# Kernel tuning notes

Hardware: AMD Instinct MI355X
Metric: run time of the kernel (lower is better)

## Reference

```python
import jax, jax.numpy as jnp
import numpy as np

B = 16384          # number of graphs
NPG = 9            # nodes per graph (op_idx reshaped to B*9)
D = 128            # d_model
L = 4              # num_layers (GCN order)
EPG = 16           # random intra-graph edges per graph
LN_EPS = 1e-5


def setup_inputs() -> dict:
    key = jax.random.key(0)
    ks = jax.random.split(key, 12)
    op_idx = jax.random.randint(ks[0], (B, NPG), 0, 7)
    # edges strictly within each 9-node graph, offset per graph
    s = jax.random.randint(ks[1], (B, EPG), 0, NPG)
    t = jax.random.randint(ks[2], (B, EPG), 0, NPG)
    off = (jnp.arange(B) * NPG)[:, None]
    src = (s + off).reshape(-1)
    dst = (t + off).reshape(-1)
    f32 = jnp.float32
    op_table = jax.random.normal(ks[3], (7, D), f32)
    device_emb = jax.random.normal(ks[4], (1, D), f32)
    Wg = jax.random.normal(ks[5], (L, D, D), f32) / np.sqrt(D)
    bg = jnp.zeros((L, D), f32)
    ln_g = jnp.ones((L, D), f32)
    ln_b = jnp.zeros((L, D), f32)
    W1 = jax.random.normal(ks[6], (L, D, 4 * D), f32) / np.sqrt(D)
    b1 = jnp.zeros((L, 4 * D), f32)
    W2 = jax.random.normal(ks[7], (L, 4 * D, D), f32) / np.sqrt(4 * D)
    b2 = jnp.zeros((L, D), f32)
    fc_w = jax.random.normal(ks[8], (D, 1), f32) / np.sqrt(D)
    fc_b = jnp.zeros((1,), f32)
    return dict(op_table=op_table, device_emb=device_emb, Wg=Wg, bg=bg,
                ln_g=ln_g, ln_b=ln_b, W1=W1, b1=b1, W2=W2, b2=b2,
                fc_w=fc_w, fc_b=fc_b, op_idx=op_idx, src=src, dst=dst)


def _layer_norm(x, g, b):
    mu = x.mean(-1, keepdims=True)
    var = jnp.mean(jnp.square(x - mu), -1, keepdims=True)
    return (x - mu) * jax.lax.rsqrt(var + LN_EPS) * g + b


def reference(op_table, device_emb, Wg, bg, ln_g, ln_b, W1, b1, W2, b2,
              fc_w, fc_b, op_idx, src, dst):
    n_graphs = op_idx.shape[0]
    N = n_graphs * NPG
    # embedding lookup + broadcast add of device embedding: [N, D]
    h = op_table[op_idx].reshape(N, -1) + device_emb
    # add self loops
    loop = jnp.arange(N)
    s_all = jnp.concatenate([src, loop])
    d_all = jnp.concatenate([dst, loop])
    deg = jax.ops.segment_sum(jnp.ones_like(s_all, dtype=h.dtype), d_all,
                              num_segments=N)
    inv_sqrt_deg = jax.lax.rsqrt(jnp.maximum(deg, 1.0))
    enorm = (inv_sqrt_deg[s_all] * inv_sqrt_deg[d_all])[:, None]  # [E,1]
    n_layers = Wg.shape[0]
    for l in range(n_layers):
        # symmetric-normalized message passing (gather -> scale -> scatter-add)
        agg = jax.ops.segment_sum(h[s_all] * enorm, d_all, num_segments=N)
        h = jax.nn.relu(agg @ Wg[l] + bg[l])
        h = _layer_norm(h, ln_g[l], ln_b[l])
        h = h + jax.nn.relu(h @ W1[l] + b1[l]) @ W2[l] + b2[l]  # residual FFN
    # mean readout over the 9 nodes of each graph -> [B, D]
    g = h.reshape(n_graphs, NPG, -1).mean(axis=1)
    return jax.nn.sigmoid(g @ fc_w + fc_b)  # [B, 1]
```

## Files before the change

### kernel.cpp

```cpp
#include <hip/hip_runtime.h>

#define NGRAPH 16384
#define NPG    9
#define DM     128
#define NLAY   4
#define EPG    16
#define GPB    14
#define RPB    128
#define NBLK   1171
#define CBS    40
#define WPL    147456

typedef __attribute__((ext_vector_type(8))) short bf16x8;
typedef __attribute__((ext_vector_type(4))) float f32x4;
typedef __attribute__((ext_vector_type(2))) float f32x2;
typedef __attribute__((ext_vector_type(4))) unsigned int u32x4;

__device__ __forceinline__ float b2f(unsigned short u){
  union { unsigned int i; float f; } v; v.i = ((unsigned int)u) << 16; return v.f;
}
__device__ __forceinline__ unsigned short f2b(float f){
  union { float fv; unsigned int i; } v; v.fv = f;
  unsigned int r = v.i + 0x7FFFu + ((v.i >> 16) & 1u);
  return (unsigned short)(r >> 16);
}
__device__ __forceinline__ unsigned int cvt2(float lo, float hi){
  unsigned int r;
  asm("v_cvt_pk_bf16_f32 %0, %1, %2" : "=v"(r) : "v"(lo), "v"(hi));
  return r;
}
__device__ __forceinline__ float uasf(unsigned int u){
  union { unsigned int i; float f; } v; v.i = u; return v.f;
}

__device__ __forceinline__ bf16x8 ldfrag128(const unsigned short* buf, int row, int kk, int g16){
  return *(const bf16x8*)&buf[row*DM + ((kk*32 + g16*8) ^ ((row & 7) << 3))];
}
__device__ __forceinline__ f32x4 mfma16(bf16x8 a, bf16x8 b, f32x4 c){
  return __builtin_amdgcn_mfma_f32_16x16x32_bf16(a, b, c, 0, 0, 0);
}

__global__ void wtr_kernel(const float* __restrict__ Wg,
                           const float* __restrict__ W1,
                           const float* __restrict__ W2,
                           unsigned short* __restrict__ wsT){
  int idx = blockIdx.x * 256 + threadIdx.x;
  int e    = idx & 7;
  int lane = (idx >> 3) & 63;
  int f    = idx >> 9;
  int l = f / 288, s = f - l*288;
  int l15 = lane & 15, g16 = lane >> 4;
  float v;
  if (s < 32){
    int kk = s >> 3, nt = s & 7;
    v = Wg[l*16384 + (kk*32 + g16*8 + e)*128 + nt*16 + l15];
  } else if (s < 160){
    int s2 = s - 32; int c = s2 >> 3, fi = s2 & 7;
    int kk = fi >> 1, nt = fi & 1;
    v = W1[l*65536 + (kk*32 + g16*8 + e)*512 + c*32 + nt*16 + l15];
  } else {
    int s3 = s - 160; int c = s3 >> 3, nt = s3 & 7;
    v = W2[l*65536 + (c*32 + g16*8 + e)*128 + nt*16 + l15];
  }
  wsT[f*512 + lane*8 + e] = f2b(v);
}

__global__ void __launch_bounds__(256, 2)
gcn_kernel(const float* __restrict__ op_table,
           const float* __restrict__ dev_emb,
           const float* __restrict__ bgp,
           const float* __restrict__ lngp,
           const float* __restrict__ lnbp,
           const float* __restrict__ b1p,
           const float* __restrict__ b2p,
           const float* __restrict__ fcw,
           const float* __restrict__ fcb,
           const int* __restrict__ op_idx,
           const int* __restrict__ srcA,
           const int* __restrict__ dstA,
           const unsigned short* __restrict__ wsT,
           float* __restrict__ out)
{
  __shared__ unsigned short H[RPB*DM];
  __shared__ unsigned short Cb[RPB*CBS];
  __shared__ float cntF[GPB][81];
  __shared__ float isd_s[RPB];
  __shared__ float bg_s[DM], lng_s[DM], lnb_s[DM], b2_s[DM];
  __shared__ float b1_s[4*DM];

  const int tid  = threadIdx.x;
  const int w    = tid >> 6;
  const int lane = tid & 63;
  const int g16  = lane >> 4;
  const int l15  = lane & 15;
  const int rbase = w * 32;
  const int g0 = blockIdx.x * GPB;
  const int nvalid = (NGRAPH - g0 < GPB) ? (NGRAPH - g0) : GPB;

  for (int i = tid; i < GPB*81; i += 256) (&cntF[0][0])[i] = 0.f;

  {
    int r  = tid >> 1;
    int gh = (tid & 1) * 8;
    int gi = r / NPG;
    int j  = r - gi*NPG;
    if (r < GPB*NPG && gi < nvalid) {
      int idx = op_idx[(g0 + gi)*NPG + j];
      const float4* ot = (const float4*)&op_table[idx*DM + gh*8];
      const float4* de = (const float4*)&dev_emb[gh*8];
      #pragma unroll
      for (int i = 0; i < 8; ++i){
        float4 a0 = ot[2*i], a1 = ot[2*i+1];
        float4 d0 = de[2*i], d1 = de[2*i+1];
        u32x4 o;
        o[0] = cvt2(a0.x + d0.x, a0.y + d0.y);
        o[1] = cvt2(a0.z + d0.z, a0.w + d0.w);
        o[2] = cvt2(a1.x + d1.x, a1.y + d1.y);
        o[3] = cvt2(a1.z + d1.z, a1.w + d1.w);
        int g = gh + i;
        *(u32x4*)&H[r*DM + ((g ^ (r & 7)) << 3)] = o;
      }
    } else {
      u32x4 z; z[0]=z[1]=z[2]=z[3]=0u;
      #pragma unroll
      for (int i = 0; i < 8; ++i){
        int g = gh + i;
        *(u32x4*)&H[r*DM + ((g ^ (r & 7)) << 3)] = z;
      }
    }
  }
  __syncthreads();

  if (tid < GPB && tid < nvalid) {
    float* c = cntF[tid];
    for (int e = 0; e < EPG; ++e){
      int s = srcA[(g0 + tid)*EPG + e];
      int d = dstA[(g0 + tid)*EPG + e];
      c[(s % NPG)*NPG + (d % NPG)] += 1.f;
    }
    #pragma unroll
    for (int j = 0; j < NPG; ++j) c[j*NPG + j] += 1.f;
  }
  __syncthreads();

  if (tid < RPB) {
    int gi = tid / NPG;
    if (tid < GPB*NPG && gi < nvalid) {
      int jd = tid - gi*NPG;
      float s = 0.f;
      #pragma unroll
      for (int js = 0; js < NPG; ++js) s += cntF[gi][js*NPG + jd];
      isd_s[tid] = rsqrtf(s);
    } else isd_s[tid] = 1.f;
  }
  __syncthreads();

  for (int idx = tid; idx < GPB*81; idx += 256){
    int gi = idx / 81;
    int e  = idx - gi*81;
    int js = e / 9, jd = e - js*9;
    (&cntF[0][0])[idx] *= isd_s[gi*NPG + js] * isd_s[gi*NPG + jd];
  }
  __syncthreads();

  #pragma unroll 1
  for (int l = 0; l < NLAY; ++l){
    const unsigned short* WL = wsT + l*WPL;

    if (tid < DM) {
      bg_s[tid]  = bgp [l*DM + tid];
      lng_s[tid] = lngp[l*DM + tid];
      lnb_s[tid] = lnbp[l*DM + tid];
      b2_s[tid]  = b2p [l*DM + tid];
    }
    b1_s[tid]       = b1p[l*4*DM + tid];
    b1_s[tid + 256] = b1p[l*4*DM + 256 + tid];
    {
      int gi = tid >> 4;
      int g  = tid & 15;
      if (gi < GPB) {
        f32x2 hs[NPG][4];
        #pragma unroll
        for (int j = 0; j < NPG; ++j){
          int row = gi*NPG + j;
          u32x4 hv = *(const u32x4*)&H[row*DM + ((g ^ (row & 7)) << 3)];
          #pragma unroll
          for (int i = 0; i < 4; ++i){
            f32x2 t;
            t[0] = uasf(hv[i] << 16);
            t[1] = uasf(hv[i] & 0xffff0000u);
            hs[j][i] = t;
          }
        }
        #pragma unroll
        for (int jd = 0; jd < NPG; ++jd){
          f32x2 av[4];
          #pragma unroll
          for (int i = 0; i < 4; ++i){ f32x2 z; z[0]=0.f; z[1]=0.f; av[i]=z; }
          #pragma unroll
          for (int js = 0; js < NPG; ++js){
            float c = cntF[gi][js*NPG + jd];
            f32x2 cc; cc[0]=c; cc[1]=c;
            #pragma unroll
            for (int i = 0; i < 4; ++i)
              av[i] = __builtin_elementwise_fma(cc, hs[js][i], av[i]);
          }
          int row = gi*NPG + jd;
          u32x4 o;
          #pragma unroll
          for (int i = 0; i < 4; ++i) o[i] = cvt2(av[i][0], av[i][1]);
          *(u32x4*)&H[row*DM + ((g ^ (row & 7)) << 3)] = o;
        }
      } else {
        int k2 = tid - GPB*16;
        int row = GPB*NPG + (k2 >> 4);
        int gg = k2 & 15;
        u32x4 z; z[0]=z[1]=z[2]=z[3]=0u;
        *(u32x4*)&H[row*DM + ((gg ^ (row & 7)) << 3)] = z;
      }
    }
    __syncthreads();

    {
      const bf16x8* Bf = (const bf16x8*)WL;
      f32x4 acc[2][8];
      #pragma unroll
      for (int mt = 0; mt < 2; ++mt)
        #pragma unroll
        for (int nt = 0; nt < 8; ++nt){ f32x4 z; z[0]=z[1]=z[2]=z[3]=0.f; acc[mt][nt]=z; }
      #pragma unroll 2
      for (int kk = 0; kk < 4; ++kk){
        bf16x8 a0 = ldfrag128(H, rbase + l15, kk, g16);
        bf16x8 a1 = ldfrag128(H, rbase + 16 + l15, kk, g16);
        __builtin_amdgcn_s_setprio(1);
        #pragma unroll
        for (int nt = 0; nt < 8; ++nt){
          bf16x8 bb = Bf[(kk*8 + nt)*64 + lane];
          acc[0][nt] = mfma16(a0, bb, acc[0][nt]);
          acc[1][nt] = mfma16(a1, bb, acc[1][nt]);
        }
        __builtin_amdgcn_s_setprio(0);
      }
      #pragma unroll
      for (int mt = 0; mt < 2; ++mt){
        float rs[4], rq[4];
        #pragma unroll
        for (int j = 0; j < 4; ++j){ rs[j] = 0.f; rq[j] = 0.f; }
        #pragma unroll
        for (int nt = 0; nt < 8; ++nt){
          #pragma unroll
          for (int j = 0; j < 4; ++j){
            float v = acc[mt][nt][j] + bg_s[nt*16 + l15];
            v = fmaxf(v, 0.f);
            acc[mt][nt][j] = v;
            rs[j] += v; rq[j] += v*v;
          }
        }
        #pragma unroll
        for (int j = 0; j < 4; ++j){
          #pragma unroll
          for (int mm = 1; mm < 16; mm <<= 1){
            rs[j] += __shfl_xor(rs[j], mm, 64);
            rq[j] += __shfl_xor(rq[j], mm, 64);
          }
          float mu  = rs[j] * (1.f/128.f);
          float var = rq[j] * (1.f/128.f) - mu*mu;
          rs[j] = mu;
          rq[j] = rsqrtf(var + 1e-5f);
        }
        int rowb = rbase + mt*16 + g16*4;
        #pragma unroll
        for (int nt = 0; nt < 8; ++nt){
          int col = nt*16 + l15;
          float lg = lng_s[col], lb = lnb_s[col];
          float x0 = (acc[mt][nt][0] - rs[0]) * rq[0] * lg + lb;
          float x1 = (acc[mt][nt][1] - rs[1]) * rq[1] * lg + lb;
          float x2 = (acc[mt][nt][2] - rs[2]) * rq[2] * lg + lb;
          float x3 = (acc[mt][nt][3] - rs[3]) * rq[3] * lg + lb;
          unsigned int p01 = cvt2(x0, x1);
          unsigned int p23 = cvt2(x2, x3);
          int r0 = rowb, r1 = rowb+1, r2 = rowb+2, r3 = rowb+3;
          H[r0*DM + (col ^ ((r0 & 7) << 3))] = (unsigned short)p01;
          H[r1*DM + (col ^ ((r1 & 7) << 3))] = (unsigned short)(p01 >> 16);
          H[r2*DM + (col ^ ((r2 & 7) << 3))] = (unsigned short)p23;
          H[r3*DM + (col ^ ((r3 & 7) << 3))] = (unsigned short)(p23 >> 16);
        }
      }
    }

    {
      const unsigned short* W1b = WL + 16384;
      const unsigned short* W2b = WL + 81920;

      bf16x8 xa[8];
      #pragma unroll
      for (int kk = 0; kk < 4; ++kk){
        xa[kk*2 + 0] = ldfrag128(H, rbase + l15, kk, g16);
        xa[kk*2 + 1] = ldfrag128(H, rbase + 16 + l15, kk, g16);
      }

      f32x4 c2[2][8];
      #pragma unroll
      for (int mt = 0; mt < 2; ++mt)
        #pragma unroll
        for (int nt = 0; nt < 8; ++nt){ f32x4 z; z[0]=z[1]=z[2]=z[3]=0.f; c2[mt][nt]=z; }
      #pragma unroll 1
      for (int c = 0; c < 16; ++c){
        const bf16x8* B1 = (const bf16x8*)(W1b + c*4096);
        const bf16x8* B2 = (const bf16x8*)(W2b + c*4096);
        bf16x8 b1r[8], b2r[8];
        #pragma unroll
        for (int f = 0; f < 8; ++f) b1r[f] = B1[f*64 + lane];
        #pragma unroll
        for (int f = 0; f < 8; ++f) b2r[f] = B2[f*64 + lane];

        f32x4 hc[2][2];
        #pragma unroll
        for (int mt = 0; mt < 2; ++mt)
          #pragma unroll
          for (int nt = 0; nt < 2; ++nt){ f32x4 z; z[0]=z[1]=z[2]=z[3]=0.f; hc[mt][nt]=z; }
        __builtin_amdgcn_s_setprio(1);
        #pragma unroll
        for (int kk = 0; kk < 4; ++kk){
          #pragma unroll
          for (int nt = 0; nt < 2; ++nt){
            bf16x8 bb = b1r[kk*2 + nt];
            hc[0][nt] = mfma16(xa[kk*2 + 0], bb, hc[0][nt]);
            hc[1][nt] = mfma16(xa[kk*2 + 1], bb, hc[1][nt]);
          }
        }
        __builtin_amdgcn_s_setprio(0);
        #pragma unroll
        for (int mt = 0; mt < 2; ++mt){
          int rowb = rbase + mt*16 + g16*4;
          #pragma unroll
          for (int nt = 0; nt < 2; ++nt){
            int col = nt*16 + l15;
            float bv = b1_s[c*32 + col];
            float v0 = fmaxf(hc[mt][nt][0] + bv, 0.f);
            float v1 = fmaxf(hc[mt][nt][1] + bv, 0.f);
            float v2 = fmaxf(hc[mt][nt][2] + bv, 0.f);
            float v3 = fmaxf(hc[mt][nt][3] + bv, 0.f);
            unsigned int p01 = cvt2(v0, v1);
            unsigned int p23 = cvt2(v2, v3);
            Cb[(rowb + 0)*CBS + col] = (unsigned short)p01;
            Cb[(rowb + 1)*CBS + col] = (unsigned short)(p01 >> 16);
            Cb[(rowb + 2)*CBS + col] = (unsigned short)p23;
            Cb[(rowb + 3)*CBS + col] = (unsigned short)(p23 >> 16);
          }
        }
        {
          bf16x8 a0 = *(const bf16x8*)&Cb[(rbase + l15)*CBS + g16*8];
          bf16x8 a1 = *(const bf16x8*)&Cb[(rbase + 16 + l15)*CBS + g16*8];
          __builtin_amdgcn_s_setprio(1);
          #pragma unroll
          for (int nt = 0; nt < 8; ++nt){
            c2[0][nt] = mfma16(a0, b2r[nt], c2[0][nt]);
            c2[1][nt] = mfma16(a1, b2r[nt], c2[1][nt]);
          }
          __builtin_amdgcn_s_setprio(0);
        }
      }

      #pragma unroll
      for (int mt = 0; mt < 2; ++mt){
        int rowb = rbase + mt*16 + g16*4;
        #pragma unroll
        for (int nt = 0; nt < 8; ++nt){
          int col = nt*16 + l15;
          float b2v = b2_s[col];
          int p0 = (rowb+0)*DM + (col ^ (((rowb+0) & 7) << 3));
          int p1 = (rowb+1)*DM + (col ^ (((rowb+1) & 7) << 3));
          int p2 = (rowb+2)*DM + (col ^ (((rowb+2) & 7) << 3));
          int p3 = (rowb+3)*DM + (col ^ (((rowb+3) & 7) << 3));
          float s0 = b2f(H[p0]) + c2[mt][nt][0] + b2v;
          float s1 = b2f(H[p1]) + c2[mt][nt][1] + b2v;
          float s2 = b2f(H[p2]) + c2[mt][nt][2] + b2v;
          float s3 = b2f(H[p3]) + c2[mt][nt][3] + b2v;
          unsigned int p01 = cvt2(s0, s1);
          unsigned int p23 = cvt2(s2, s3);
          H[p0] = (unsigned short)p01;
          H[p1] = (unsigned short)(p01 >> 16);
          H[p2] = (unsigned short)p23;
          H[p3] = (unsigned short)(p23 >> 16);
        }
      }
    }
    __syncthreads();
  }

  {
    int gi = tid >> 4;
    int g  = tid & 15;
    if (gi < nvalid) {
      float m[8];
      #pragma unroll
      for (int i = 0; i < 8; ++i) m[i] = 0.f;
      #pragma unroll
      for (int j = 0; j < NPG; ++j){
        int row = gi*NPG + j;
        bf16x8 hv = *(const bf16x8*)&H[row*DM + ((g ^ (row & 7)) << 3)];
        #pragma unroll
        for (int i = 0; i < 8; ++i) m[i] += b2f((unsigned short)hv[i]);
      }
      const float4* fw = (const float4*)&fcw[g*8];
      float4 w0 = fw[0], w1 = fw[1];
      float dot = m[0]*w0.x + m[1]*w0.y + m[2]*w0.z + m[3]*w0.w
                + m[4]*w1.x + m[5]*w1.y + m[6]*w1.z + m[7]*w1.w;
      dot *= (1.f/9.f);
      #pragma unroll
      for (int mm = 1; mm < 16; mm <<= 1) dot += __shfl_xor(dot, mm, 64);
      if ((tid & 15) == 0){
        float z = dot + fcb[0];
        out[g0 + gi] = 1.f / (1.f + __expf(-z));
      }
    }
  }
}

extern "C" void kernel_launch(void* const* d_in, const int* in_sizes, int n_in,
                              void* d_out, int out_size, void* d_ws, size_t ws_size,
                              hipStream_t stream)
{
  const float* op_table = (const float*)d_in[0];
  const float* dev_emb  = (const float*)d_in[1];
  const float* Wg  = (const float*)d_in[2];
  const float* bg  = (const float*)d_in[3];
  const float* lng = (const float*)d_in[4];
  const float* lnb = (const float*)d_in[5];
  const float* W1  = (const float*)d_in[6];
  const float* b1  = (const float*)d_in[7];
  const float* W2  = (const float*)d_in[8];
  const float* b2  = (const float*)d_in[9];
  const float* fcw = (const float*)d_in[10];
  const float* fcb = (const float*)d_in[11];
  const int* op_idx = (const int*)d_in[12];
  const int* srcA   = (const int*)d_in[13];
  const int* dstA   = (const int*)d_in[14];
  unsigned short* wsT = (unsigned short*)d_ws;

  wtr_kernel<<<2304, 256, 0, stream>>>(Wg, W1, W2, wsT);
  gcn_kernel<<<NBLK, 256, 0, stream>>>(op_table, dev_emb, bg, lng, lnb, b1, b2,
                                       fcw, fcb, op_idx, srcA, dstA, wsT,
                                       (float*)d_out);
}
```

Baseline: 275.6 us.

## Prefetch layer weights into registers and double-buffer W1 chunks across FFN loop

Global loads of the GCN weight fragments are hoisted to the top of each layer, before the aggregation phase and barrier, so their latency overlaps the message-passing work. The FFN loop is unrolled by two, with W1 fragments double-buffered in registers (the even and odd chunks). The next chunk's W1 is loaded while the current chunk computes, and the first W1 chunk is prefetched during the LayerNorm epilogue. This raises register pressure considerably (32 extra bf16x8 for Wg plus 16 for W1), which could reduce occupancy or cause spills.

```diff
diff --git a/kernel.cpp b/kernel.cpp
--- a/kernel.cpp
+++ b/kernel.cpp
@@ -166,6 +166,11 @@
   #pragma unroll 1
   for (int l = 0; l < NLAY; ++l){
     const unsigned short* WL = wsT + l*WPL;
+    const bf16x8* Bg = (const bf16x8*)WL;
+
+    bf16x8 wg01[16];
+    #pragma unroll
+    for (int f = 0; f < 16; ++f) wg01[f] = Bg[f*64 + lane];
 
     if (tid < DM) {
       bg_s[tid]  = bgp [l*DM + tid];
@@ -221,26 +226,48 @@
     }
     __syncthreads();
 
+    bf16x8 b1E[8], b1O[8];
     {
-      const bf16x8* Bf = (const bf16x8*)WL;
+      bf16x8 wg23[16];
+      #pragma unroll
+      for (int f = 0; f < 16; ++f) wg23[f] = Bg[(16 + f)*64 + lane];
+
       f32x4 acc[2][8];
       #pragma unroll
       for (int mt = 0; mt < 2; ++mt)
         #pragma unroll
         for (int nt = 0; nt < 8; ++nt){ f32x4 z; z[0]=z[1]=z[2]=z[3]=0.f; acc[mt][nt]=z; }
-      #pragma unroll 2
-      for (int kk = 0; kk < 4; ++kk){
+      #pragma unroll
+      for (int kk = 0; kk < 2; ++kk){
         bf16x8 a0 = ldfrag128(H, rbase + l15, kk, g16);
         bf16x8 a1 = ldfrag128(H, rbase + 16 + l15, kk, g16);
         __builtin_amdgcn_s_setprio(1);
         #pragma unroll
         for (int nt = 0; nt < 8; ++nt){
-          bf16x8 bb = Bf[(kk*8 + nt)*64 + lane];
-          acc[0][nt] = mfma16(a0, bb, acc[0][nt]);
-          acc[1][nt] = mfma16(a1, bb, acc[1][nt]);
+          acc[0][nt] = mfma16(a0, wg01[kk*8 + nt], acc[0][nt]);
+          acc[1][nt] = mfma16(a1, wg01[kk*8 + nt], acc[1][nt]);
         }
         __builtin_amdgcn_s_setprio(0);
       }
+      #pragma unroll
+      for (int kk = 0; kk < 2; ++kk){
+        bf16x8 a0 = ldfrag128(H, rbase + l15, 2 + kk, g16);
+        bf16x8 a1 = ldfrag128(H, rbase + 16 + l15, 2 + kk, g16);
+        __builtin_amdgcn_s_setprio(1);
+        #pragma unroll
+        for (int nt = 0; nt < 8; ++nt){
+          acc[0][nt] = mfma16(a0, wg23[kk*8 + nt], acc[0][nt]);
+          acc[1][nt] = mfma16(a1, wg23[kk*8 + nt], acc[1][nt]);
+        }
+        __builtin_amdgcn_s_setprio(0);
+      }
+
+      {
+        const bf16x8* B1 = (const bf16x8*)(WL + 16384);
+        #pragma unroll
+        for (int f = 0; f < 8; ++f) b1E[f] = B1[f*64 + lane];
+      }
+
       #pragma unroll
       for (int mt = 0; mt < 2; ++mt){
         float rs[4], rq[4];
@@ -304,63 +331,86 @@
       for (int mt = 0; mt < 2; ++mt)
         #pragma unroll
         for (int nt = 0; nt < 8; ++nt){ f32x4 z; z[0]=z[1]=z[2]=z[3]=0.f; c2[mt][nt]=z; }
+
+      bf16x8 b2r[8];
+      f32x4 hc[2][2];
+
+#define FFN_CHUNK(B1CUR, CIDX)                                              \
+      {                                                                     \
+        __builtin_amdgcn_s_setprio(1);                                      \
+        _Pragma("unroll")                                                   \
+        for (int mt = 0; mt < 2; ++mt)                                      \
+          _Pragma("unroll")                                                 \
+          for (int nt = 0; nt < 2; ++nt){                                   \
+            f32x4 z; z[0]=z[1]=z[2]=z[3]=0.f; hc[mt][nt]=z;                 \
+          }                                                                 \
+        _Pragma("unroll")                                                   \
+        for (int kk = 0; kk < 4; ++kk){                                     \
+          _Pragma("unroll")                                                 \
+          for (int nt = 0; nt < 2; ++nt){                                   \
+            bf16x8 bb = B1CUR[kk*2 + nt];                                   \
+            hc[0][nt] = mfma16(xa[kk*2 + 0], bb, hc[0][nt]);                \
+            hc[1][nt] = mfma16(xa[kk*2 + 1], bb, hc[1][nt]);                \
+          }                                                                 \
+        }                                                                   \
+        __builtin_amdgcn_s_setprio(0);                                      \
+        _Pragma("unroll")                                                   \
+        for (int mt = 0; mt < 2; ++mt){                                     \
+          int rowb = rbase + mt*16 + g16*4;                                 \
+          _Pragma("unroll")                                                 \
+          for (int nt = 0; nt < 2; ++nt){                                   \
+            int col = nt*16 + l15;                                          \
+            float bv = b1_s[(CIDX)*32 + col];                               \
+            float v0 = fmaxf(hc[mt][nt][0] + bv, 0.f);                      \
+            float v1 = fmaxf(hc[mt][nt][1] + bv, 0.f);                      \
+            float v2 = fmaxf(hc[mt][nt][2] + bv, 0.f);                      \
+            float v3 = fmaxf(hc[mt][nt][3] + bv, 0.f);                      \
+            unsigned int q01 = cvt2(v0, v1);                                \
+            unsigned int q23 = cvt2(v2, v3);                                \
+            Cb[(rowb + 0)*CBS + col] = (unsigned short)q01;                 \
+            Cb[(rowb + 1)*CBS + col] = (unsigned short)(q01 >> 16);         \
+            Cb[(rowb + 2)*CBS + col] = (unsigned short)q23;                 \
+            Cb[(rowb + 3)*CBS + col] = (unsigned short)(q23 >> 16);         \
+          }                                                                 \
+        }                                                                   \
+        {                                                                   \
+          bf16x8 a0 = *(const bf16x8*)&Cb[(rbase + l15)*CBS + g16*8];       \
+          bf16x8 a1 = *(const bf16x8*)&Cb[(rbase + 16 + l15)*CBS + g16*8];  \
+          __builtin_amdgcn_s_setprio(1);                                    \
+          _Pragma("unroll")                                                 \
+          for (int nt = 0; nt < 8; ++nt){                                   \
+            c2[0][nt] = mfma16(a0, b2r[nt], c2[0][nt]);                     \
+            c2[1][nt] = mfma16(a1, b2r[nt], c2[1][nt]);                     \
+          }                                                                 \
+          __builtin_amdgcn_s_setprio(0);                                    \
+        }                                                                   \
+      }
+
       #pragma unroll 1
-      for (int c = 0; c < 16; ++c){
-        const bf16x8* B1 = (const bf16x8*)(W1b + c*4096);
-        const bf16x8* B2 = (const bf16x8*)(W2b + c*4096);
-        bf16x8 b1r[8], b2r[8];
-        #pragma unroll
-        for (int f = 0; f < 8; ++f) b1r[f] = B1[f*64 + lane];
-        #pragma unroll
-        for (int f = 0; f < 8; ++f) b2r[f] = B2[f*64 + lane];
-
-        f32x4 hc[2][2];
-        #pragma unroll
-        for (int mt = 0; mt < 2; ++mt)
-          #pragma unroll
-          for (int nt = 0; nt < 2; ++nt){ f32x4 z; z[0]=z[1]=z[2]=z[3]=0.f; hc[mt][nt]=z; }
-        __builtin_amdgcn_s_setprio(1);
-        #pragma unroll
-        for (int kk = 0; kk < 4; ++kk){
-          #pragma unroll
-          for (int nt = 0; nt < 2; ++nt){
-            bf16x8 bb = b1r[kk*2 + nt];
-            hc[0][nt] = mfma16(xa[kk*2 + 0], bb, hc[0][nt]);
-            hc[1][nt] = mfma16(xa[kk*2 + 1], bb, hc[1][nt]);
+      for (int cc = 0; cc < 8; ++cc){
+        int c0 = 2*cc, c1 = 2*cc + 1;
+        {
+          const bf16x8* B2 = (const bf16x8*)(W2b + c0*4096);
+          #pragma unroll
+          for (int f = 0; f < 8; ++f) b2r[f] = B2[f*64 + lane];
+          const bf16x8* B1n = (const bf16x8*)(W1b + c1*4096);
+          #pragma unroll
+          for (int f = 0; f < 8; ++f) b1O[f] = B1n[f*64 + lane];
+          FFN_CHUNK(b1E, c0);
+        }
+        {
+          const bf16x8* B2 = (const bf16x8*)(W2b + c1*4096);
+          #pragma unroll
+          for (int f = 0; f < 8; ++f) b2r[f] = B2[f*64 + lane];
+          if (cc < 7){
+            const bf16x8* B1n = (const bf16x8*)(W1b + (c1+1)*4096);
+            #pragma unroll
+            for (int f = 0; f < 8; ++f) b1E[f] = B1n[f*64 + lane];
           }
-        }
-        __builtin_amdgcn_s_setprio(0);
-        #pragma unroll
-        for (int mt = 0; mt < 2; ++mt){
-          int rowb = rbase + mt*16 + g16*4;
-          #pragma unroll
-          for (int nt = 0; nt < 2; ++nt){
-            int col = nt*16 + l15;
-            float bv = b1_s[c*32 + col];
-            float v0 = fmaxf(hc[mt][nt][0] + bv, 0.f);
-            float v1 = fmaxf(hc[mt][nt][1] + bv, 0.f);
-            float v2 = fmaxf(hc[mt][nt][2] + bv, 0.f);
-            float v3 = fmaxf(hc[mt][nt][3] + bv, 0.f);
-            unsigned int p01 = cvt2(v0, v1);
-            unsigned int p23 = cvt2(v2, v3);
-            Cb[(rowb + 0)*CBS + col] = (unsigned short)p01;
-            Cb[(rowb + 1)*CBS + col] = (unsigned short)(p01 >> 16);
-            Cb[(rowb + 2)*CBS + col] = (unsigned short)p23;
-            Cb[(rowb + 3)*CBS + col] = (unsigned short)(p23 >> 16);
-          }
-        }
-        {
-          bf16x8 a0 = *(const bf16x8*)&Cb[(rbase + l15)*CBS + g16*8];
-          bf16x8 a1 = *(const bf16x8*)&Cb[(rbase + 16 + l15)*CBS + g16*8];
-          __builtin_amdgcn_s_setprio(1);
-          #pragma unroll
-          for (int nt = 0; nt < 8; ++nt){
-            c2[0][nt] = mfma16(a0, b2r[nt], c2[0][nt]);
-            c2[1][nt] = mfma16(a1, b2r[nt], c2[1][nt]);
-          }
-          __builtin_amdgcn_s_setprio(0);
-        }
-      }
+          FFN_CHUNK(b1O, c1);
+        }
+      }
+#undef FFN_CHUNK
 
       #pragma unroll
       for (int mt = 0; mt < 2; ++mt){
```

Result: slower. 340.0 us (+23.4%).

## Align graphs to wavefront row slices to drop per-layer block barriers

Applied to the files above, without the earlier changes.

Reassigns graphs so each wavefront owns three whole 9-node graphs within its own 32-row slice of H. The aggregation, GEMMs and FFN for a layer then only touch rows the wavefront owns, so the per-layer __syncthreads calls are removed and all layers' bias and LayerNorm parameters are preloaded once into shared memory. The cost is fewer graphs per block (12 instead of 14), which means more blocks and some wasted padded rows per wave. Rows 27-31 of each wave are never zeroed after the initial load, so they rely on the initial zero fill staying benign through the layers.

```diff
diff --git a/kernel.cpp b/kernel.cpp
--- a/kernel.cpp
+++ b/kernel.cpp
@@ -5,9 +5,9 @@
 #define DM     128
 #define NLAY   4
 #define EPG    16
-#define GPB    14
+#define GPB    12
 #define RPB    128
-#define NBLK   1171
+#define NBLK   1366
 #define CBS    40
 #define WPL    147456
 
@@ -84,9 +84,9 @@
   __shared__ unsigned short H[RPB*DM];
   __shared__ unsigned short Cb[RPB*CBS];
   __shared__ float cntF[GPB][81];
-  __shared__ float isd_s[RPB];
-  __shared__ float bg_s[DM], lng_s[DM], lnb_s[DM], b2_s[DM];
-  __shared__ float b1_s[4*DM];
+  __shared__ float isd_s[GPB*NPG];
+  __shared__ float bg_s[NLAY*DM], lng_s[NLAY*DM], lnb_s[NLAY*DM], b2_s[NLAY*DM];
+  __shared__ float b1_s[NLAY*4*DM];
 
   const int tid  = threadIdx.x;
   const int w    = tid >> 6;
@@ -98,14 +98,22 @@
   const int nvalid = (NGRAPH - g0 < GPB) ? (NGRAPH - g0) : GPB;
 
   for (int i = tid; i < GPB*81; i += 256) (&cntF[0][0])[i] = 0.f;
+  for (int i = tid; i < NLAY*DM; i += 256){
+    bg_s[i]  = bgp[i];
+    lng_s[i] = lngp[i];
+    lnb_s[i] = lnbp[i];
+    b2_s[i]  = b2p[i];
+  }
+  for (int i = tid; i < NLAY*4*DM; i += 256) b1_s[i] = b1p[i];
 
   {
     int r  = tid >> 1;
     int gh = (tid & 1) * 8;
-    int gi = r / NPG;
-    int j  = r - gi*NPG;
-    if (r < GPB*NPG && gi < nvalid) {
-      int idx = op_idx[(g0 + gi)*NPG + j];
+    int wv = r >> 5, lr = r & 31;
+    int gl = lr / 9, j = lr - gl*9;
+    int gidx = wv*3 + gl;
+    if (lr < 27 && gidx < nvalid) {
+      int idx = op_idx[(g0 + gidx)*NPG + j];
       const float4* ot = (const float4*)&op_table[idx*DM + gh*8];
       const float4* de = (const float4*)&dev_emb[gh*8];
       #pragma unroll
@@ -143,23 +151,23 @@
   }
   __syncthreads();
 
-  if (tid < RPB) {
-    int gi = tid / NPG;
-    if (tid < GPB*NPG && gi < nvalid) {
-      int jd = tid - gi*NPG;
+  if (tid < GPB*NPG) {
+    int gl = tid / NPG;
+    if (gl < nvalid) {
+      int jd = tid - gl*NPG;
       float s = 0.f;
       #pragma unroll
-      for (int js = 0; js < NPG; ++js) s += cntF[gi][js*NPG + jd];
+      for (int js = 0; js < NPG; ++js) s += cntF[gl][js*NPG + jd];
       isd_s[tid] = rsqrtf(s);
     } else isd_s[tid] = 1.f;
   }
   __syncthreads();
 
   for (int idx = tid; idx < GPB*81; idx += 256){
-    int gi = idx / 81;
-    int e  = idx - gi*81;
+    int gl = idx / 81;
+    int e  = idx - gl*81;
     int js = e / 9, jd = e - js*9;
-    (&cntF[0][0])[idx] *= isd_s[gi*NPG + js] * isd_s[gi*NPG + jd];
+    (&cntF[0][0])[idx] *= isd_s[gl*NPG + js] * isd_s[gl*NPG + jd];
   }
   __syncthreads();
 
@@ -167,22 +175,16 @@
   for (int l = 0; l < NLAY; ++l){
     const unsigned short* WL = wsT + l*WPL;
 
-    if (tid < DM) {
-      bg_s[tid]  = bgp [l*DM + tid];
-      lng_s[tid] = lngp[l*DM + tid];
-      lnb_s[tid] = lnbp[l*DM + tid];
-      b2_s[tid]  = b2p [l*DM + tid];
-    }
-    b1_s[tid]       = b1p[l*4*DM + tid];
-    b1_s[tid + 256] = b1p[l*4*DM + 256 + tid];
     {
-      int gi = tid >> 4;
-      int g  = tid & 15;
-      if (gi < GPB) {
+      int gi_l = g16;
+      int g    = l15;
+      if (gi_l < 3) {
+        int gl = w*3 + gi_l;
+        int rb = rbase + gi_l*9;
         f32x2 hs[NPG][4];
         #pragma unroll
         for (int j = 0; j < NPG; ++j){
-          int row = gi*NPG + j;
+          int row = rb + j;
           u32x4 hv = *(const u32x4*)&H[row*DM + ((g ^ (row & 7)) << 3)];
           #pragma unroll
           for (int i = 0; i < 4; ++i){
@@ -199,27 +201,20 @@
           for (int i = 0; i < 4; ++i){ f32x2 z; z[0]=0.f; z[1]=0.f; av[i]=z; }
           #pragma unroll
           for (int js = 0; js < NPG; ++js){
-            float c = cntF[gi][js*NPG + jd];
+            float c = cntF[gl][js*NPG + jd];
             f32x2 cc; cc[0]=c; cc[1]=c;
             #pragma unroll
             for (int i = 0; i < 4; ++i)
               av[i] = __builtin_elementwise_fma(cc, hs[js][i], av[i]);
           }
-          int row = gi*NPG + jd;
+          int row = rb + jd;
           u32x4 o;
           #pragma unroll
           for (int i = 0; i < 4; ++i) o[i] = cvt2(av[i][0], av[i][1]);
           *(u32x4*)&H[row*DM + ((g ^ (row & 7)) << 3)] = o;
         }
-      } else {
-        int k2 = tid - GPB*16;
-        int row = GPB*NPG + (k2 >> 4);
-        int gg = k2 & 15;
-        u32x4 z; z[0]=z[1]=z[2]=z[3]=0u;
-        *(u32x4*)&H[row*DM + ((gg ^ (row & 7)) << 3)] = z;
-      }
-    }
-    __syncthreads();
+      }
+    }
 
     {
       const bf16x8* Bf = (const bf16x8*)WL;
@@ -250,7 +245,7 @@
         for (int nt = 0; nt < 8; ++nt){
           #pragma unroll
           for (int j = 0; j < 4; ++j){
-            float v = acc[mt][nt][j] + bg_s[nt*16 + l15];
+            float v = acc[mt][nt][j] + bg_s[l*DM + nt*16 + l15];
             v = fmaxf(v, 0.f);
             acc[mt][nt][j] = v;
             rs[j] += v; rq[j] += v*v;
@@ -272,7 +267,7 @@
         #pragma unroll
         for (int nt = 0; nt < 8; ++nt){
           int col = nt*16 + l15;
-          float lg = lng_s[col], lb = lnb_s[col];
+          float lg = lng_s[l*DM + col], lb = lnb_s[l*DM + col];
           float x0 = (acc[mt][nt][0] - rs[0]) * rq[0] * lg + lb;
           float x1 = (acc[mt][nt][1] - rs[1]) * rq[1] * lg + lb;
           float x2 = (acc[mt][nt][2] - rs[2]) * rq[2] * lg + lb;
@@ -336,7 +331,7 @@
           #pragma unroll
           for (int nt = 0; nt < 2; ++nt){
             int col = nt*16 + l15;
-            float bv = b1_s[c*32 + col];
+            float bv = b1_s[l*4*DM + c*32 + col];
             float v0 = fmaxf(hc[mt][nt][0] + bv, 0.f);
             float v1 = fmaxf(hc[mt][nt][1] + bv, 0.f);
             float v2 = fmaxf(hc[mt][nt][2] + bv, 0.f);
@@ -368,7 +363,7 @@
         #pragma unroll
         for (int nt = 0; nt < 8; ++nt){
           int col = nt*16 + l15;
-          float b2v = b2_s[col];
+          float b2v = b2_s[l*DM + col];
           int p0 = (rowb+0)*DM + (col ^ (((rowb+0) & 7) << 3));
           int p1 = (rowb+1)*DM + (col ^ (((rowb+1) & 7) << 3));
           int p2 = (rowb+2)*DM + (col ^ (((rowb+2) & 7) << 3));
@@ -386,19 +381,21 @@
         }
       }
     }
-    __syncthreads();
-  }
+  }
+
+  __syncthreads();
 
   {
     int gi = tid >> 4;
     int g  = tid & 15;
-    if (gi < nvalid) {
+    if (gi < GPB && gi < nvalid) {
+      int rb = (gi/3)*32 + (gi - (gi/3)*3)*9;
       float m[8];
       #pragma unroll
       for (int i = 0; i < 8; ++i) m[i] = 0.f;
       #pragma unroll
       for (int j = 0; j < NPG; ++j){
-        int row = gi*NPG + j;
+        int row = rb + j;
         bf16x8 hv = *(const bf16x8*)&H[row*DM + ((g ^ (row & 7)) << 3)];
         #pragma unroll
         for (int i = 0; i < 8; ++i) m[i] += b2f((unsigned short)hv[i]);
```

After: 300.8 us. 9.1% more time.
